# Performance work log

Measured on AMD Instinct MI355X. Metric: run time of the kernel, lower is better.

## Reference

```python
import jax, jax.numpy as jnp
import numpy as np

B, N, F_IN = 1, 4096, 128
H, F_OUT = 8, 64
NEG = -1e9


def setup_inputs() -> dict:
    key = jax.random.key(0)
    ks = jax.random.split(key, 7)
    x = jax.random.normal(ks[0], (B, N, F_IN), dtype=jnp.float32)
    edge = jax.random.uniform(ks[1], (N, N)) < 0.02
    edge = edge | jnp.eye(N, dtype=bool)
    adj = jnp.where(edge, 0.0, NEG).astype(jnp.float32)
    # Glorot-uniform params
    def glorot(k, shape, fan_in, fan_out):
        lim = float(np.sqrt(6.0 / (fan_in + fan_out)))
        return jax.random.uniform(k, shape, jnp.float32, -lim, lim)
    W_proj = glorot(ks[2], (H * F_OUT, F_IN), F_IN, H * F_OUT)      # linear_proj.weight
    a_src = glorot(ks[3], (1, H, F_OUT), H, F_OUT)                   # scoring_fn_source
    a_tgt = glorot(ks[4], (1, H, F_OUT), H, F_OUT)                   # scoring_fn_target
    W_skip = glorot(ks[5], (H * F_OUT, F_IN), F_IN, H * F_OUT)       # skip_proj.weight
    bias = jnp.zeros((H * F_OUT,), dtype=jnp.float32)
    return {"in_nodes_features": x, "adj": adj, "W_proj": W_proj,
            "a_src": a_src, "a_tgt": a_tgt, "W_skip": W_skip, "bias": bias}


def reference(in_nodes_features, adj, W_proj, a_src, a_tgt, W_skip, bias):
    x = in_nodes_features                                  # [B,N,Fin]  (dropout p=0)
    proj = jnp.einsum('bnf,of->bno', x, W_proj)            # [B,N,H*Fo]
    proj = proj.reshape(B, N, H, F_OUT)                    # [B,N,H,Fo]
    s_src = jnp.einsum('bnhd,xhd->bhn', proj, a_src)       # [B,H,N] (row / source)
    s_tgt = jnp.einsum('bnhd,xhd->bhn', proj, a_tgt)       # [B,H,N] (col / target)
    scores = s_src[:, :, :, None] + s_tgt[:, :, None, :]   # [B,H,N,N]
    scores = jax.nn.leaky_relu(scores, negative_slope=0.2)
    att = jax.nn.softmax(scores + adj, axis=-1)            # adj additive mask, broadcast over B,H
    out = jnp.einsum('bhij,bjhd->bihd', att, proj)         # [B,N,H,Fo]
    out = out + jnp.einsum('bnf,of->bno', x, W_skip).reshape(B, N, H, F_OUT)  # skip (dims differ)
    out = out.reshape(B, N, H * F_OUT) + bias              # concat + bias
    out = jax.nn.elu(out)                                  # activation ELU
    return out, adj
```

## Files before the change

### kernel.cpp

```cpp
#include <hip/hip_runtime.h>
#include <cmath>

#define N_NODES 4096
#define FIN     128
#define H_HEADS 8
#define FOUT    64
#define HF      512

__global__ __launch_bounds__(256) void gemm_proj_skip(
    const float* __restrict__ x, const float* __restrict__ Wp,
    const float* __restrict__ Ws, float* __restrict__ proj,
    float* __restrict__ skip)
{
    __shared__ __align__(16) float AsT[64][68];
    __shared__ __align__(16) float BsT[64][68];

    const int t  = threadIdx.x;
    const int rb = blockIdx.y * 64;
    const int cb = blockIdx.x * 64;
    const float* Wbase = (cb < HF) ? (Wp + cb * FIN) : (Ws + (cb - HF) * FIN);
    float* dst = (cb < HF) ? (proj + cb) : (skip + (cb - HF));

    const int tx = t & 15;
    const int ty = t >> 4;
    float acc[4][4] = {{0.f}};

    for (int kb = 0; kb < FIN; kb += 64) {
        #pragma unroll
        for (int p = 0; p < 4; ++p) {
            int f4 = t + p * 256;
            int r  = f4 >> 4;
            int k4 = f4 & 15;
            float4 a = *(const float4*)(x + (size_t)(rb + r) * FIN + kb + k4 * 4);
            AsT[k4*4+0][r] = a.x; AsT[k4*4+1][r] = a.y;
            AsT[k4*4+2][r] = a.z; AsT[k4*4+3][r] = a.w;
            float4 b = *(const float4*)(Wbase + (size_t)r * FIN + kb + k4 * 4);
            BsT[k4*4+0][r] = b.x; BsT[k4*4+1][r] = b.y;
            BsT[k4*4+2][r] = b.z; BsT[k4*4+3][r] = b.w;
        }
        __syncthreads();
        #pragma unroll 8
        for (int kk = 0; kk < 64; ++kk) {
            float4 a = *(const float4*)&AsT[kk][ty * 4];
            float4 b = *(const float4*)&BsT[kk][tx * 4];
            acc[0][0] += a.x*b.x; acc[0][1] += a.x*b.y; acc[0][2] += a.x*b.z; acc[0][3] += a.x*b.w;
            acc[1][0] += a.y*b.x; acc[1][1] += a.y*b.y; acc[1][2] += a.y*b.z; acc[1][3] += a.y*b.w;
            acc[2][0] += a.z*b.x; acc[2][1] += a.z*b.y; acc[2][2] += a.z*b.z; acc[2][3] += a.z*b.w;
            acc[3][0] += a.w*b.x; acc[3][1] += a.w*b.y; acc[3][2] += a.w*b.z; acc[3][3] += a.w*b.w;
        }
        __syncthreads();
    }
    #pragma unroll
    for (int i = 0; i < 4; ++i) {
        float4 v = make_float4(acc[i][0], acc[i][1], acc[i][2], acc[i][3]);
        *(float4*)(dst + (size_t)(rb + ty * 4 + i) * HF + tx * 4) = v;
    }
}

__global__ __launch_bounds__(256) void score_kernel(
    const float* __restrict__ proj, const float* __restrict__ a_src,
    const float* __restrict__ a_tgt, float* __restrict__ s_src,
    float* __restrict__ s_tgt)
{
    const int wave = threadIdx.x >> 6;
    const int lane = threadIdx.x & 63;
    const int n = blockIdx.x * 4 + wave;
    const float* pr = proj + (size_t)n * HF;
    #pragma unroll
    for (int h = 0; h < H_HEADS; ++h) {
        float v  = pr[h * FOUT + lane];
        float vs = v * a_src[h * FOUT + lane];
        float vt = v * a_tgt[h * FOUT + lane];
        #pragma unroll
        for (int off = 32; off; off >>= 1) {
            vs += __shfl_down(vs, off);
            vt += __shfl_down(vt, off);
        }
        if (lane == 0) {
            s_src[h * N_NODES + n] = vs;
            s_tgt[h * N_NODES + n] = vt;
        }
    }
}

#define CAP 512

__global__ __launch_bounds__(512) void att_kernel(
    const float* __restrict__ adj, const float* __restrict__ proj,
    const float* __restrict__ skip, const float* __restrict__ s_src,
    const float* __restrict__ s_tgt, const float* __restrict__ bias,
    float* __restrict__ out, float* __restrict__ adj_out)
{
    __shared__ int   s_idx[CAP];
    __shared__ float sp[H_HEADS][CAP];
    __shared__ int   s_cnt;

    const int t = threadIdx.x;
    const int i = blockIdx.x;
    if (t == 0) s_cnt = 0;
    __syncthreads();

    const float4* arow = (const float4*)(adj + (size_t)i * N_NODES);
    float4*       aout = (float4*)(adj_out + (size_t)i * N_NODES);
    #pragma unroll
    for (int it = 0; it < 2; ++it) {
        int f4 = t + it * 512;
        float4 v = arow[f4];
        aout[f4] = v;
        int j0 = f4 * 4;
        if (v.x == 0.0f) { int p = atomicAdd(&s_cnt, 1); if (p < CAP) s_idx[p] = j0;     }
        if (v.y == 0.0f) { int p = atomicAdd(&s_cnt, 1); if (p < CAP) s_idx[p] = j0 + 1; }
        if (v.z == 0.0f) { int p = atomicAdd(&s_cnt, 1); if (p < CAP) s_idx[p] = j0 + 2; }
        if (v.w == 0.0f) { int p = atomicAdd(&s_cnt, 1); if (p < CAP) s_idx[p] = j0 + 3; }
    }
    __syncthreads();
    const int c = (s_cnt < CAP) ? s_cnt : CAP;

    for (int k = t; k < c; k += 512) {
        int j = s_idx[k];
        #pragma unroll
        for (int h = 0; h < H_HEADS; ++h) {
            float e = s_src[h * N_NODES + i] + s_tgt[h * N_NODES + j];
            e = (e > 0.0f) ? e : 0.2f * e;
            sp[h][k] = e;
        }
    }
    __syncthreads();

    const int h    = t >> 6;
    const int lane = t & 63;
    float m = -1e30f;
    for (int k = lane; k < c; k += 64) m = fmaxf(m, sp[h][k]);
    #pragma unroll
    for (int off = 32; off; off >>= 1) m = fmaxf(m, __shfl_xor(m, off));
    float l = 0.0f;
    for (int k = lane; k < c; k += 64) {
        float e = __expf(sp[h][k] - m);
        sp[h][k] = e;
        l += e;
    }
    #pragma unroll
    for (int off = 32; off; off >>= 1) l += __shfl_xor(l, off);
    const float inv = 1.0f / l;

    float acc = 0.0f;
    const float* projh = proj + h * FOUT + lane;
    int k = 0;
    for (; k + 4 <= c; k += 4) {
        int   j0 = s_idx[k],     j1 = s_idx[k + 1], j2 = s_idx[k + 2], j3 = s_idx[k + 3];
        float p0 = sp[h][k],     p1 = sp[h][k + 1], p2 = sp[h][k + 2], p3 = sp[h][k + 3];
        float v0 = projh[(size_t)j0 * HF];
        float v1 = projh[(size_t)j1 * HF];
        float v2 = projh[(size_t)j2 * HF];
        float v3 = projh[(size_t)j3 * HF];
        acc += p0 * v0; acc += p1 * v1; acc += p2 * v2; acc += p3 * v3;
    }
    for (; k < c; ++k) acc += sp[h][k] * projh[(size_t)s_idx[k] * HF];

    const int o = h * FOUT + lane;
    float res = acc * inv + skip[(size_t)i * HF + o] + bias[o];
    res = (res > 0.0f) ? res : expm1f(res);
    out[(size_t)i * HF + o] = res;
}

extern "C" void kernel_launch(void* const* d_in, const int* in_sizes, int n_in,
                              void* d_out, int out_size, void* d_ws, size_t ws_size,
                              hipStream_t stream)
{
    const float* x     = (const float*)d_in[0];
    const float* adj   = (const float*)d_in[1];
    const float* Wp    = (const float*)d_in[2];
    const float* a_src = (const float*)d_in[3];
    const float* a_tgt = (const float*)d_in[4];
    const float* Ws    = (const float*)d_in[5];
    const float* bias  = (const float*)d_in[6];

    float* out     = (float*)d_out;
    float* adj_out = out + (size_t)N_NODES * HF;

    float* proj = (float*)d_ws;
    float* ssrc = proj + (size_t)N_NODES * HF;
    float* stgt = ssrc + (size_t)H_HEADS * N_NODES;
    float* skip = out;

    gemm_proj_skip<<<dim3(16, 64), 256, 0, stream>>>(x, Wp, Ws, proj, skip);
    score_kernel<<<N_NODES / 4, 256, 0, stream>>>(proj, a_src, a_tgt, ssrc, stgt);
    att_kernel<<<N_NODES, 512, 0, stream>>>(adj, proj, skip, ssrc, stgt, bias,
                                            out, adj_out);
}
```

Measured before the change: 216.8 us.

## Fuse score computation into GEMM, store proj as bf16, vectorize aggregation gather

The score kernel is folded into the projection GEMM epilogue, which computes per-head source and target scores with shuffle reductions, removing one launch and a reread of proj. Proj is stored as bf16 to halve gather traffic in the attention kernel, and each lane now reads 8 bf16 values with a 16-byte load, followed by a cross-group shuffle reduction. Score layout changes to node-major so the 8 heads load as two float4, adj copy uses nontemporal loads and stores, and the neighbour cap drops to 256 to save shared memory. Trade-offs: bf16 loses precision on proj, and rows with more than 256 neighbours would be truncated.

```diff
diff --git a/kernel.cpp b/kernel.cpp
--- a/kernel.cpp
+++ b/kernel.cpp
@@ -6,11 +6,23 @@
 #define H_HEADS 8
 #define FOUT    64
 #define HF      512
-
-__global__ __launch_bounds__(256) void gemm_proj_skip(
+#define CAP     256
+
+typedef float  vf4 __attribute__((ext_vector_type(4)));
+typedef unsigned int vu4 __attribute__((ext_vector_type(4)));
+
+__device__ __forceinline__ unsigned short f2bf(float f) {
+    unsigned u = __float_as_uint(f);
+    u += 0x7fff + ((u >> 16) & 1);
+    return (unsigned short)(u >> 16);
+}
+
+__global__ __launch_bounds__(256) void gemm_fused(
     const float* __restrict__ x, const float* __restrict__ Wp,
-    const float* __restrict__ Ws, float* __restrict__ proj,
-    float* __restrict__ skip)
+    const float* __restrict__ Ws, const float* __restrict__ a_src,
+    const float* __restrict__ a_tgt,
+    unsigned short* __restrict__ proj, float* __restrict__ skip,
+    float* __restrict__ ssrc, float* __restrict__ stgt)
 {
     __shared__ __align__(16) float AsT[64][68];
     __shared__ __align__(16) float BsT[64][68];
@@ -18,8 +30,8 @@
     const int t  = threadIdx.x;
     const int rb = blockIdx.y * 64;
     const int cb = blockIdx.x * 64;
-    const float* Wbase = (cb < HF) ? (Wp + cb * FIN) : (Ws + (cb - HF) * FIN);
-    float* dst = (cb < HF) ? (proj + cb) : (skip + (cb - HF));
+    const bool isP = (cb < HF);
+    const float* Wbase = isP ? (Wp + cb * FIN) : (Ws + (cb - HF) * FIN);
 
     const int tx = t & 15;
     const int ty = t >> 4;
@@ -50,63 +62,68 @@
         }
         __syncthreads();
     }
-    #pragma unroll
-    for (int i = 0; i < 4; ++i) {
-        float4 v = make_float4(acc[i][0], acc[i][1], acc[i][2], acc[i][3]);
-        *(float4*)(dst + (size_t)(rb + ty * 4 + i) * HF + tx * 4) = v;
-    }
-}
-
-__global__ __launch_bounds__(256) void score_kernel(
-    const float* __restrict__ proj, const float* __restrict__ a_src,
-    const float* __restrict__ a_tgt, float* __restrict__ s_src,
-    float* __restrict__ s_tgt)
-{
-    const int wave = threadIdx.x >> 6;
-    const int lane = threadIdx.x & 63;
-    const int n = blockIdx.x * 4 + wave;
-    const float* pr = proj + (size_t)n * HF;
-    #pragma unroll
-    for (int h = 0; h < H_HEADS; ++h) {
-        float v  = pr[h * FOUT + lane];
-        float vs = v * a_src[h * FOUT + lane];
-        float vt = v * a_tgt[h * FOUT + lane];
-        #pragma unroll
-        for (int off = 32; off; off >>= 1) {
-            vs += __shfl_down(vs, off);
-            vt += __shfl_down(vt, off);
-        }
-        if (lane == 0) {
-            s_src[h * N_NODES + n] = vs;
-            s_tgt[h * N_NODES + n] = vt;
-        }
-    }
-}
-
-#define CAP 512
+
+    if (isP) {
+        #pragma unroll
+        for (int i = 0; i < 4; ++i) {
+            ushort4 v;
+            v.x = f2bf(acc[i][0]); v.y = f2bf(acc[i][1]);
+            v.z = f2bf(acc[i][2]); v.w = f2bf(acc[i][3]);
+            *(ushort4*)(proj + (size_t)(rb + ty*4 + i) * HF + cb + tx * 4) = v;
+        }
+        const int h = cb >> 6;
+        const float as0 = a_src[cb + tx*4 + 0], as1 = a_src[cb + tx*4 + 1];
+        const float as2 = a_src[cb + tx*4 + 2], as3 = a_src[cb + tx*4 + 3];
+        const float at0 = a_tgt[cb + tx*4 + 0], at1 = a_tgt[cb + tx*4 + 1];
+        const float at2 = a_tgt[cb + tx*4 + 2], at3 = a_tgt[cb + tx*4 + 3];
+        #pragma unroll
+        for (int i = 0; i < 4; ++i) {
+            float ps = acc[i][0]*as0 + acc[i][1]*as1 + acc[i][2]*as2 + acc[i][3]*as3;
+            float pt = acc[i][0]*at0 + acc[i][1]*at1 + acc[i][2]*at2 + acc[i][3]*at3;
+            #pragma unroll
+            for (int off = 1; off < 16; off <<= 1) {
+                ps += __shfl_xor(ps, off);
+                pt += __shfl_xor(pt, off);
+            }
+            if (tx == 0) {
+                int n = rb + ty*4 + i;
+                ssrc[n * H_HEADS + h] = ps;
+                stgt[n * H_HEADS + h] = pt;
+            }
+        }
+    } else {
+        #pragma unroll
+        for (int i = 0; i < 4; ++i) {
+            float4 v = make_float4(acc[i][0], acc[i][1], acc[i][2], acc[i][3]);
+            *(float4*)(skip + (size_t)(rb + ty*4 + i) * HF + (cb - HF) + tx * 4) = v;
+        }
+    }
+}
 
 __global__ __launch_bounds__(512) void att_kernel(
-    const float* __restrict__ adj, const float* __restrict__ proj,
-    const float* __restrict__ skip, const float* __restrict__ s_src,
-    const float* __restrict__ s_tgt, const float* __restrict__ bias,
+    const float* __restrict__ adj, const unsigned short* __restrict__ proj,
+    const float* __restrict__ skip, const float* __restrict__ ssrc,
+    const float* __restrict__ stgt, const float* __restrict__ bias,
     float* __restrict__ out, float* __restrict__ adj_out)
 {
     __shared__ int   s_idx[CAP];
     __shared__ float sp[H_HEADS][CAP];
+    __shared__ float s_i[H_HEADS];
     __shared__ int   s_cnt;
 
     const int t = threadIdx.x;
     const int i = blockIdx.x;
     if (t == 0) s_cnt = 0;
+    if (t < H_HEADS) s_i[t] = ssrc[i * H_HEADS + t];
     __syncthreads();
 
-    const float4* arow = (const float4*)(adj + (size_t)i * N_NODES);
-    float4*       aout = (float4*)(adj_out + (size_t)i * N_NODES);
+    const vf4* arow = (const vf4*)(adj + (size_t)i * N_NODES);
+    vf4*       aout = (vf4*)(adj_out + (size_t)i * N_NODES);
     #pragma unroll
     for (int it = 0; it < 2; ++it) {
         int f4 = t + it * 512;
-        float4 v = arow[f4];
-        aout[f4] = v;
+        vf4 v = __builtin_nontemporal_load(arow + f4);
+        __builtin_nontemporal_store(v, aout + f4);
         int j0 = f4 * 4;
         if (v.x == 0.0f) { int p = atomicAdd(&s_cnt, 1); if (p < CAP) s_idx[p] = j0;     }
         if (v.y == 0.0f) { int p = atomicAdd(&s_cnt, 1); if (p < CAP) s_idx[p] = j0 + 1; }
@@ -118,12 +135,18 @@
 
     for (int k = t; k < c; k += 512) {
         int j = s_idx[k];
-        #pragma unroll
-        for (int h = 0; h < H_HEADS; ++h) {
-            float e = s_src[h * N_NODES + i] + s_tgt[h * N_NODES + j];
-            e = (e > 0.0f) ? e : 0.2f * e;
-            sp[h][k] = e;
-        }
+        const float* st = stgt + j * H_HEADS;
+        float4 t0 = *(const float4*)(st);
+        float4 t1 = *(const float4*)(st + 4);
+        float e;
+        e = s_i[0] + t0.x; sp[0][k] = (e > 0.f) ? e : 0.2f * e;
+        e = s_i[1] + t0.y; sp[1][k] = (e > 0.f) ? e : 0.2f * e;
+        e = s_i[2] + t0.z; sp[2][k] = (e > 0.f) ? e : 0.2f * e;
+        e = s_i[3] + t0.w; sp[3][k] = (e > 0.f) ? e : 0.2f * e;
+        e = s_i[4] + t1.x; sp[4][k] = (e > 0.f) ? e : 0.2f * e;
+        e = s_i[5] + t1.y; sp[5][k] = (e > 0.f) ? e : 0.2f * e;
+        e = s_i[6] + t1.z; sp[6][k] = (e > 0.f) ? e : 0.2f * e;
+        e = s_i[7] + t1.w; sp[7][k] = (e > 0.f) ? e : 0.2f * e;
     }
     __syncthreads();
 
@@ -143,24 +166,44 @@
     for (int off = 32; off; off >>= 1) l += __shfl_xor(l, off);
     const float inv = 1.0f / l;
 
-    float acc = 0.0f;
-    const float* projh = proj + h * FOUT + lane;
-    int k = 0;
-    for (; k + 4 <= c; k += 4) {
-        int   j0 = s_idx[k],     j1 = s_idx[k + 1], j2 = s_idx[k + 2], j3 = s_idx[k + 3];
-        float p0 = sp[h][k],     p1 = sp[h][k + 1], p2 = sp[h][k + 2], p3 = sp[h][k + 3];
-        float v0 = projh[(size_t)j0 * HF];
-        float v1 = projh[(size_t)j1 * HF];
-        float v2 = projh[(size_t)j2 * HF];
-        float v3 = projh[(size_t)j3 * HF];
-        acc += p0 * v0; acc += p1 * v1; acc += p2 * v2; acc += p3 * v3;
-    }
-    for (; k < c; ++k) acc += sp[h][k] * projh[(size_t)s_idx[k] * HF];
-
-    const int o = h * FOUT + lane;
-    float res = acc * inv + skip[(size_t)i * HF + o] + bias[o];
-    res = (res > 0.0f) ? res : expm1f(res);
-    out[(size_t)i * HF + o] = res;
+    const int g  = lane >> 3;
+    const int k8 = lane & 7;
+    float a8[8] = {0.f, 0.f, 0.f, 0.f, 0.f, 0.f, 0.f, 0.f};
+    const unsigned short* pbase = proj + h * FOUT + k8 * 8;
+    #pragma unroll 2
+    for (int k = g; k < c; k += 8) {
+        int   j = s_idx[k];
+        float p = sp[h][k];
+        vu4 raw = *(const vu4*)(pbase + (size_t)j * HF);
+        a8[0] += p * __uint_as_float(raw.x << 16);
+        a8[1] += p * __uint_as_float(raw.x & 0xffff0000u);
+        a8[2] += p * __uint_as_float(raw.y << 16);
+        a8[3] += p * __uint_as_float(raw.y & 0xffff0000u);
+        a8[4] += p * __uint_as_float(raw.z << 16);
+        a8[5] += p * __uint_as_float(raw.z & 0xffff0000u);
+        a8[6] += p * __uint_as_float(raw.w << 16);
+        a8[7] += p * __uint_as_float(raw.w & 0xffff0000u);
+    }
+    #pragma unroll
+    for (int off = 8; off < 64; off <<= 1) {
+        #pragma unroll
+        for (int q = 0; q < 8; ++q) a8[q] += __shfl_xor(a8[q], off);
+    }
+    if (g == 0) {
+        const int o = h * FOUT + k8 * 8;
+        const float* sk = skip + (size_t)i * HF + o;
+        const float* bs = bias + o;
+        float r[8];
+        #pragma unroll
+        for (int q = 0; q < 8; ++q) {
+            float v = a8[q] * inv + sk[q] + bs[q];
+            r[q] = (v > 0.f) ? v : expm1f(v);
+        }
+        float4 w0 = make_float4(r[0], r[1], r[2], r[3]);
+        float4 w1 = make_float4(r[4], r[5], r[6], r[7]);
+        *(float4*)(out + (size_t)i * HF + o)     = w0;
+        *(float4*)(out + (size_t)i * HF + o + 4) = w1;
+    }
 }
 
 extern "C" void kernel_launch(void* const* d_in, const int* in_sizes, int n_in,
@@ -178,13 +221,13 @@
     float* out     = (float*)d_out;
     float* adj_out = out + (size_t)N_NODES * HF;
 
-    float* proj = (float*)d_ws;
-    float* ssrc = proj + (size_t)N_NODES * HF;
-    float* stgt = ssrc + (size_t)H_HEADS * N_NODES;
+    unsigned short* proj = (unsigned short*)d_ws;
+    float* ssrc = (float*)((char*)d_ws + (size_t)N_NODES * HF * sizeof(unsigned short));
+    float* stgt = ssrc + (size_t)N_NODES * H_HEADS;
     float* skip = out;
 
-    gemm_proj_skip<<<dim3(16, 64), 256, 0, stream>>>(x, Wp, Ws, proj, skip);
-    score_kernel<<<N_NODES / 4, 256, 0, stream>>>(proj, a_src, a_tgt, ssrc, stgt);
+    gemm_fused<<<dim3(16, 64), 256, 0, stream>>>(x, Wp, Ws, a_src, a_tgt,
+                                                 proj, skip, ssrc, stgt);
     att_kernel<<<N_NODES, 512, 0, stream>>>(adj, proj, skip, ssrc, stgt, bias,
                                             out, adj_out);
 }
```

New measurement: 193.9 us. 10.6% less time.
